# Kernel tuning notes

Hardware: AMD Instinct MI355X
Metric: run time of the kernel (lower is better)

## Reference

```python
import jax, jax.numpy as jnp
import numpy as np

N_NODES = 100000
N_EDGES = 1600000
DIM = 128
N_LAYERS = 3
N_GRAPHS = 512
BN_EPS = 1e-5


def setup_inputs() -> dict:
    key = jax.random.key(0)
    ks = jax.random.split(key, 8)
    x = jax.random.normal(ks[0], (N_NODES, DIM), dtype=jnp.float32)
    edge_index = jax.random.randint(ks[1], (2, N_EDGES), 0, N_NODES)
    batch = jnp.sort(jax.random.randint(ks[2], (N_NODES,), 0, N_GRAPHS))
    s = 1.0 / np.sqrt(DIM).astype(np.float32)
    # GIN MLP per layer: Linear(DIM->DIM), ReLU, Linear(DIM->DIM); stacked over layers
    W1 = jax.random.normal(ks[3], (N_LAYERS, DIM, DIM), dtype=jnp.float32) * s
    b1 = jnp.zeros((N_LAYERS, DIM), jnp.float32)
    W2 = jax.random.normal(ks[4], (N_LAYERS, DIM, DIM), dtype=jnp.float32) * s
    b2 = jnp.zeros((N_LAYERS, DIM), jnp.float32)
    # BatchNorm1d affine params
    gamma = jnp.ones((N_LAYERS, DIM), jnp.float32)
    beta = jnp.zeros((N_LAYERS, DIM), jnp.float32)
    return dict(x=x, edge_index=edge_index, batch=batch,
                W1=W1, b1=b1, W2=W2, b2=b2, gamma=gamma, beta=beta)


def reference(x, edge_index, batch, W1, b1, W2, b2, gamma, beta):
    src, dst = edge_index[0], edge_index[1]
    n = x.shape[0]
    z = x
    zs = []
    for l in range(N_LAYERS):
        # GINConv (eps=0): h_i = MLP((1+eps)*z_i + sum_{j in N(i)} z_j)
        agg = jax.ops.segment_sum(z[src], dst, num_segments=n)  # scatter-add messages
        h = agg + z
        h = jnp.maximum(h @ W1[l] + b1[l], 0.0) @ W2[l] + b2[l]
        h = jnp.maximum(h, 0.0)  # F.relu
        # BatchNorm1d (training-mode batch statistics, biased variance)
        mu = h.mean(axis=0)
        var = h.var(axis=0)
        z = (h - mu) * jax.lax.rsqrt(var + BN_EPS) * gamma[l] + beta[l]
        zs.append(z)
    gs = [jax.ops.segment_sum(zl, batch, num_segments=N_GRAPHS) for zl in zs]
    z_out = jnp.concatenate(zs, axis=1)   # [N, L*DIM]
    g_out = jnp.concatenate(gs, axis=1)   # [G, L*DIM]
    return (z_out, g_out)
```

## Files before the change

### kernel.cpp

```cpp
#include <hip/hip_runtime.h>

#define N_NODES 100000
#define N_EDGES 1600000
#define DIM 128
#define NLAYERS 3
#define NGRAPHS 512
#define BN_EPS 1e-5f

#define RT 64
#define KC 32
#define XP 36
#define WP 132
#define HP 132

#define SCHUNK 512
#define SBLOCKS ((N_NODES + SCHUNK - 1) / SCHUNK)

__global__ __launch_bounds__(256) void hist_kernel(const int* __restrict__ dst,
                                                   int* __restrict__ deg) {
  for (int e = blockIdx.x * blockDim.x + threadIdx.x; e < N_EDGES;
       e += gridDim.x * blockDim.x)
    atomicAdd(&deg[dst[e]], 1);
}

__global__ __launch_bounds__(256) void partial_kernel(const int* __restrict__ deg,
                                                      int* __restrict__ bsum) {
  __shared__ int red[256];
  const int t = threadIdx.x;
  const int i0 = blockIdx.x * SCHUNK + 2 * t;
  int s = 0;
  if (i0 + 1 < N_NODES) {
    const int2 v = *(const int2*)(deg + i0);
    s = v.x + v.y;
  } else if (i0 < N_NODES) {
    s = deg[i0];
  }
  red[t] = s;
  __syncthreads();
  for (int off = 128; off > 0; off >>= 1) {
    if (t < off) red[t] += red[t + off];
    __syncthreads();
  }
  if (t == 0) bsum[blockIdx.x] = red[0];
}

__global__ __launch_bounds__(256) void bscan_kernel(const int* __restrict__ bsum,
                                                    int* __restrict__ boff,
                                                    int* __restrict__ row_ptr) {
  __shared__ int s[256];
  const int t = threadIdx.x;
  const int v = (t < SBLOCKS) ? bsum[t] : 0;
  s[t] = v;
  __syncthreads();
  for (int off = 1; off < 256; off <<= 1) {
    int u = (t >= off) ? s[t - off] : 0;
    __syncthreads();
    s[t] += u;
    __syncthreads();
  }
  if (t < SBLOCKS) boff[t] = s[t] - v;
  if (t == SBLOCKS - 1) row_ptr[N_NODES] = s[t];
}

__global__ __launch_bounds__(256) void emit_kernel(const int* __restrict__ deg,
                                                   const int* __restrict__ boff,
                                                   int* __restrict__ row_ptr,
                                                   int* __restrict__ cursor) {
  __shared__ int s[256];
  const int t = threadIdx.x;
  const int i0 = blockIdx.x * SCHUNK + 2 * t;
  int d0 = 0, d1 = 0;
  if (i0 + 1 < N_NODES) {
    const int2 v = *(const int2*)(deg + i0);
    d0 = v.x; d1 = v.y;
  } else if (i0 < N_NODES) {
    d0 = deg[i0];
  }
  const int pair = d0 + d1;
  s[t] = pair;
  __syncthreads();
  for (int off = 1; off < 256; off <<= 1) {
    int u = (t >= off) ? s[t - off] : 0;
    __syncthreads();
    s[t] += u;
    __syncthreads();
  }
  const int base = boff[blockIdx.x] + s[t] - pair;
  if (i0 + 1 < N_NODES) {
    const int2 rp = make_int2(base, base + d0);
    *(int2*)(row_ptr + i0) = rp;
    *(int2*)(cursor + i0) = rp;
  } else if (i0 < N_NODES) {
    row_ptr[i0] = base;
    cursor[i0] = base;
  }
}

__global__ __launch_bounds__(256) void fill_kernel(const int* __restrict__ src,
                                                   const int* __restrict__ dst,
                                                   int* __restrict__ cursor,
                                                   int* __restrict__ col) {
  for (int e = blockIdx.x * blockDim.x + threadIdx.x; e < N_EDGES;
       e += gridDim.x * blockDim.x) {
    const int d = dst[e];
    const int pos = atomicAdd(&cursor[d], 1);
    col[pos] = src[e];
  }
}

__global__ __launch_bounds__(256) void agg_kernel(const float* __restrict__ zin,
                                                  int zstride,
                                                  const int* __restrict__ row_ptr,
                                                  const int* __restrict__ col,
                                                  float* __restrict__ agg) {
  const int w = (blockIdx.x * 256 + threadIdx.x) >> 6;
  const int lane = threadIdx.x & 63;
  if (w >= N_NODES) return;
  const int start = row_ptr[w];
  const int end = row_ptr[w + 1];

  float2 acc = ((const float2*)(zin + (size_t)w * zstride))[lane];
  int j = start;
  for (; j + 8 <= end; j += 8) {
    const int c0 = col[j], c1 = col[j + 1], c2 = col[j + 2], c3 = col[j + 3];
    const int c4 = col[j + 4], c5 = col[j + 5], c6 = col[j + 6], c7 = col[j + 7];
    const float2 v0 = ((const float2*)(zin + (size_t)c0 * zstride))[lane];
    const float2 v1 = ((const float2*)(zin + (size_t)c1 * zstride))[lane];
    const float2 v2 = ((const float2*)(zin + (size_t)c2 * zstride))[lane];
    const float2 v3 = ((const float2*)(zin + (size_t)c3 * zstride))[lane];
    const float2 v4 = ((const float2*)(zin + (size_t)c4 * zstride))[lane];
    const float2 v5 = ((const float2*)(zin + (size_t)c5 * zstride))[lane];
    const float2 v6 = ((const float2*)(zin + (size_t)c6 * zstride))[lane];
    const float2 v7 = ((const float2*)(zin + (size_t)c7 * zstride))[lane];
    acc.x += ((v0.x + v1.x) + (v2.x + v3.x)) + ((v4.x + v5.x) + (v6.x + v7.x));
    acc.y += ((v0.y + v1.y) + (v2.y + v3.y)) + ((v4.y + v5.y) + (v6.y + v7.y));
  }
  for (; j + 4 <= end; j += 4) {
    const int c0 = col[j], c1 = col[j + 1], c2 = col[j + 2], c3 = col[j + 3];
    const float2 v0 = ((const float2*)(zin + (size_t)c0 * zstride))[lane];
    const float2 v1 = ((const float2*)(zin + (size_t)c1 * zstride))[lane];
    const float2 v2 = ((const float2*)(zin + (size_t)c2 * zstride))[lane];
    const float2 v3 = ((const float2*)(zin + (size_t)c3 * zstride))[lane];
    acc.x += (v0.x + v1.x) + (v2.x + v3.x);
    acc.y += (v0.y + v1.y) + (v2.y + v3.y);
  }
  for (; j < end; ++j) {
    const int c = col[j];
    const float2 v = ((const float2*)(zin + (size_t)c * zstride))[lane];
    acc.x += v.x;
    acc.y += v.y;
  }
  ((float2*)(agg + (size_t)w * DIM))[lane] = acc;
}

__global__ __launch_bounds__(256) void mlp_kernel(
    const float* __restrict__ X,
    const float* __restrict__ W1, const float* __restrict__ b1,
    const float* __restrict__ W2, const float* __restrict__ b2,
    float* __restrict__ out,
    int lcol,
    float* __restrict__ bnsum) {
  __shared__ float smem[32 * WP + RT * HP];
  float* Ws = smem;
  float* Xs = smem + 32 * WP;
  float* Hs = smem + 32 * WP;
  float* red = smem + 32 * WP;

  const int tid = threadIdx.x;
  const int cg = tid & 15, rg = tid >> 4;
  const int c0 = cg * 8, r0 = rg * 4;
  const int n0 = blockIdx.x * RT;

  float4 acc[4][2];
#pragma unroll
  for (int rr = 0; rr < 4; ++rr) {
    acc[rr][0] = make_float4(0.f, 0.f, 0.f, 0.f);
    acc[rr][1] = make_float4(0.f, 0.f, 0.f, 0.f);
  }

  for (int kc = 0; kc < DIM / KC; ++kc) {
    const int k0 = kc * KC;
    __syncthreads();
    {
      const int kk = tid >> 3, q = tid & 7;
      const float4* s = (const float4*)(W1 + (size_t)(k0 + kk) * DIM + q * 16);
      float4* d = (float4*)(Ws + kk * WP + q * 16);
      d[0] = s[0]; d[1] = s[1]; d[2] = s[2]; d[3] = s[3];
    }
    {
      const int i = tid >> 2, q = tid & 3;
      const int n = n0 + i;
      float4 v0 = make_float4(0, 0, 0, 0), v1 = v0;
      if (n < N_NODES) {
        const float4* s = (const float4*)(X + (size_t)n * DIM + k0 + q * 8);
        v0 = s[0]; v1 = s[1];
      }
      float4* d = (float4*)(Xs + i * XP + q * 8);
      d[0] = v0; d[1] = v1;
    }
    __syncthreads();
#pragma unroll 8
    for (int kk = 0; kk < KC; ++kk) {
      const float4 wA = *(const float4*)(Ws + kk * WP + c0);
      const float4 wB = *(const float4*)(Ws + kk * WP + c0 + 4);
#pragma unroll
      for (int rr = 0; rr < 4; ++rr) {
        const float a = Xs[(r0 + rr) * XP + kk];
        acc[rr][0].x = fmaf(a, wA.x, acc[rr][0].x);
        acc[rr][0].y = fmaf(a, wA.y, acc[rr][0].y);
        acc[rr][0].z = fmaf(a, wA.z, acc[rr][0].z);
        acc[rr][0].w = fmaf(a, wA.w, acc[rr][0].w);
        acc[rr][1].x = fmaf(a, wB.x, acc[rr][1].x);
        acc[rr][1].y = fmaf(a, wB.y, acc[rr][1].y);
        acc[rr][1].z = fmaf(a, wB.z, acc[rr][1].z);
        acc[rr][1].w = fmaf(a, wB.w, acc[rr][1].w);
      }
    }
  }

  const float4 b1A = *(const float4*)(b1 + c0);
  const float4 b1B = *(const float4*)(b1 + c0 + 4);
  __syncthreads();
#pragma unroll
  for (int rr = 0; rr < 4; ++rr) {
    float4 hA, hB;
    hA.x = fmaxf(acc[rr][0].x + b1A.x, 0.f);
    hA.y = fmaxf(acc[rr][0].y + b1A.y, 0.f);
    hA.z = fmaxf(acc[rr][0].z + b1A.z, 0.f);
    hA.w = fmaxf(acc[rr][0].w + b1A.w, 0.f);
    hB.x = fmaxf(acc[rr][1].x + b1B.x, 0.f);
    hB.y = fmaxf(acc[rr][1].y + b1B.y, 0.f);
    hB.z = fmaxf(acc[rr][1].z + b1B.z, 0.f);
    hB.w = fmaxf(acc[rr][1].w + b1B.w, 0.f);
    *(float4*)(Hs + (r0 + rr) * HP + c0) = hA;
    *(float4*)(Hs + (r0 + rr) * HP + c0 + 4) = hB;
    acc[rr][0] = make_float4(0.f, 0.f, 0.f, 0.f);
    acc[rr][1] = make_float4(0.f, 0.f, 0.f, 0.f);
  }

  for (int kc = 0; kc < DIM / KC; ++kc) {
    const int k0 = kc * KC;
    __syncthreads();
    {
      const int kk = tid >> 3, q = tid & 7;
      const float4* s = (const float4*)(W2 + (size_t)(k0 + kk) * DIM + q * 16);
      float4* d = (float4*)(Ws + kk * WP + q * 16);
      d[0] = s[0]; d[1] = s[1]; d[2] = s[2]; d[3] = s[3];
    }
    __syncthreads();
#pragma unroll 8
    for (int kk = 0; kk < KC; ++kk) {
      const float4 wA = *(const float4*)(Ws + kk * WP + c0);
      const float4 wB = *(const float4*)(Ws + kk * WP + c0 + 4);
#pragma unroll
      for (int rr = 0; rr < 4; ++rr) {
        const float a = Hs[(r0 + rr) * HP + k0 + kk];
        acc[rr][0].x = fmaf(a, wA.x, acc[rr][0].x);
        acc[rr][0].y = fmaf(a, wA.y, acc[rr][0].y);
        acc[rr][0].z = fmaf(a, wA.z, acc[rr][0].z);
        acc[rr][0].w = fmaf(a, wA.w, acc[rr][0].w);
        acc[rr][1].x = fmaf(a, wB.x, acc[rr][1].x);
        acc[rr][1].y = fmaf(a, wB.y, acc[rr][1].y);
        acc[rr][1].z = fmaf(a, wB.z, acc[rr][1].z);
        acc[rr][1].w = fmaf(a, wB.w, acc[rr][1].w);
      }
    }
  }

  const float4 b2A = *(const float4*)(b2 + c0);
  const float4 b2B = *(const float4*)(b2 + c0 + 4);
  float s[8], q2[8];
#pragma unroll
  for (int cc = 0; cc < 8; ++cc) { s[cc] = 0.f; q2[cc] = 0.f; }
#pragma unroll
  for (int rr = 0; rr < 4; ++rr) {
    const int n = n0 + r0 + rr;
    float4 hA, hB;
    hA.x = fmaxf(acc[rr][0].x + b2A.x, 0.f);
    hA.y = fmaxf(acc[rr][0].y + b2A.y, 0.f);
    hA.z = fmaxf(acc[rr][0].z + b2A.z, 0.f);
    hA.w = fmaxf(acc[rr][0].w + b2A.w, 0.f);
    hB.x = fmaxf(acc[rr][1].x + b2B.x, 0.f);
    hB.y = fmaxf(acc[rr][1].y + b2B.y, 0.f);
    hB.z = fmaxf(acc[rr][1].z + b2B.z, 0.f);
    hB.w = fmaxf(acc[rr][1].w + b2B.w, 0.f);
    if (n < N_NODES) {
      *(float4*)(out + (size_t)n * (NLAYERS * DIM) + lcol + c0) = hA;
      *(float4*)(out + (size_t)n * (NLAYERS * DIM) + lcol + c0 + 4) = hB;
      s[0] += hA.x; s[1] += hA.y; s[2] += hA.z; s[3] += hA.w;
      s[4] += hB.x; s[5] += hB.y; s[6] += hB.z; s[7] += hB.w;
      q2[0] += hA.x * hA.x; q2[1] += hA.y * hA.y;
      q2[2] += hA.z * hA.z; q2[3] += hA.w * hA.w;
      q2[4] += hB.x * hB.x; q2[5] += hB.y * hB.y;
      q2[6] += hB.z * hB.z; q2[7] += hB.w * hB.w;
    }
  }
  __syncthreads();
#pragma unroll
  for (int cc = 0; cc < 8; ++cc) red[rg * 128 + c0 + cc] = s[cc];
  __syncthreads();
  if (tid < 128) {
    float t = 0.f;
#pragma unroll
    for (int g = 0; g < 16; ++g) t += red[g * 128 + tid];
    unsafeAtomicAdd(&bnsum[tid], t);
  }
  __syncthreads();
#pragma unroll
  for (int cc = 0; cc < 8; ++cc) red[rg * 128 + c0 + cc] = q2[cc];
  __syncthreads();
  if (tid < 128) {
    float t = 0.f;
#pragma unroll
    for (int g = 0; g < 16; ++g) t += red[g * 128 + tid];
    unsafeAtomicAdd(&bnsum[128 + tid], t);
  }
}

__global__ __launch_bounds__(128) void bn_finalize_kernel(
    const float* __restrict__ bnsum, const float* __restrict__ gamma,
    const float* __restrict__ beta, float* __restrict__ bnfin) {
  const int c = threadIdx.x;
  const float inv_n = 1.f / (float)N_NODES;
  const float mu = bnsum[c] * inv_n;
  const float var = bnsum[128 + c] * inv_n - mu * mu;
  const float inv = rsqrtf(var + BN_EPS);
  const float sc = gamma[c] * inv;
  bnfin[c] = sc;
  bnfin[128 + c] = beta[c] - mu * sc;
}

__global__ __launch_bounds__(256) void bn_norm_kernel(float* __restrict__ zcol,
                                                      const float* __restrict__ bnfin) {
  const int idx = blockIdx.x * 256 + threadIdx.x;
  if (idx >= N_NODES * 32) return;
  const int n = idx >> 5, c4 = idx & 31;
  const float4 sc = ((const float4*)bnfin)[c4];
  const float4 sh = ((const float4*)(bnfin + 128))[c4];
  float4* p = (float4*)(zcol + (size_t)n * (NLAYERS * DIM)) + c4;
  float4 v = *p;
  v.x = fmaf(v.x, sc.x, sh.x);
  v.y = fmaf(v.y, sc.y, sh.y);
  v.z = fmaf(v.z, sc.z, sh.z);
  v.w = fmaf(v.w, sc.w, sh.w);
  *p = v;
}

__global__ __launch_bounds__(128) void pool_kernel(const float* __restrict__ zout,
                                                   const int* __restrict__ batch,
                                                   float* __restrict__ gout) {
  const int g = blockIdx.x / 3;
  const int chunk = blockIdx.x % 3;
  const int c = chunk * 128 + threadIdx.x;
  int lo = 0, hi = N_NODES;
  while (lo < hi) {
    const int m = (lo + hi) >> 1;
    if (batch[m] < g) lo = m + 1; else hi = m;
  }
  int lo2 = lo, hi2 = N_NODES;
  while (lo2 < hi2) {
    const int m = (lo2 + hi2) >> 1;
    if (batch[m] < g + 1) lo2 = m + 1; else hi2 = m;
  }
  float acc = 0.f;
  for (int n = lo; n < lo2; ++n) acc += zout[(size_t)n * (NLAYERS * DIM) + c];
  gout[(size_t)g * (NLAYERS * DIM) + c] = acc;
}

extern "C" void kernel_launch(void* const* d_in, const int* in_sizes, int n_in,
                              void* d_out, int out_size, void* d_ws, size_t ws_size,
                              hipStream_t stream) {
  const float* x = (const float*)d_in[0];
  const int* ei = (const int*)d_in[1];
  const int* src = ei;
  const int* dst = ei + N_EDGES;
  const int* batch = (const int*)d_in[2];
  const float* W1 = (const float*)d_in[3];
  const float* b1 = (const float*)d_in[4];
  const float* W2 = (const float*)d_in[5];
  const float* b2 = (const float*)d_in[6];
  const float* gamma = (const float*)d_in[7];
  const float* beta = (const float*)d_in[8];
  float* out = (float*)d_out;
  float* gout = out + (size_t)N_NODES * NLAYERS * DIM;

  char* ws = (char*)d_ws;
  size_t off = 0;
  auto alloc = [&](size_t bytes) -> void* {
    off = (off + 511) & ~(size_t)511;
    void* p = ws + off;
    off += bytes;
    return p;
  };
  int* row_ptr = (int*)alloc((N_NODES + 1) * sizeof(int));
  int* cursor = (int*)alloc(N_NODES * sizeof(int));
  int* deg = (int*)alloc(N_NODES * sizeof(int));
  int* col = (int*)alloc(N_EDGES * sizeof(int));
  int* bsum = (int*)alloc(SBLOCKS * sizeof(int));
  int* boff = (int*)alloc(SBLOCKS * sizeof(int));
  float* agg = (float*)alloc((size_t)N_NODES * DIM * sizeof(float));
  float* bnsum = (float*)alloc(NLAYERS * 256 * sizeof(float));
  float* bnfin = (float*)alloc(NLAYERS * 256 * sizeof(float));

  hipMemsetAsync(deg, 0, N_NODES * sizeof(int), stream);
  hipMemsetAsync(bnsum, 0, NLAYERS * 256 * sizeof(float), stream);

  hist_kernel<<<2048, 256, 0, stream>>>(dst, deg);
  partial_kernel<<<SBLOCKS, 256, 0, stream>>>(deg, bsum);
  bscan_kernel<<<1, 256, 0, stream>>>(bsum, boff, row_ptr);
  emit_kernel<<<SBLOCKS, 256, 0, stream>>>(deg, boff, row_ptr, cursor);
  fill_kernel<<<2048, 256, 0, stream>>>(src, dst, cursor, col);

  for (int l = 0; l < NLAYERS; ++l) {
    const float* zin = (l == 0) ? x : (out + (size_t)(l - 1) * DIM);
    const int zstride = (l == 0) ? DIM : NLAYERS * DIM;
    agg_kernel<<<(N_NODES * 64 + 255) / 256, 256, 0, stream>>>(zin, zstride,
                                                               row_ptr, col, agg);
    mlp_kernel<<<(N_NODES + RT - 1) / RT, 256, 0, stream>>>(
        agg, W1 + (size_t)l * DIM * DIM, b1 + (size_t)l * DIM,
        W2 + (size_t)l * DIM * DIM, b2 + (size_t)l * DIM, out, l * DIM,
        bnsum + l * 256);
    bn_finalize_kernel<<<1, 128, 0, stream>>>(bnsum + l * 256, gamma + l * DIM,
                                              beta + l * DIM, bnfin + l * 256);
    bn_norm_kernel<<<(N_NODES * 32 + 255) / 256, 256, 0, stream>>>(
        out + (size_t)l * DIM, bnfin + l * 256);
  }
  pool_kernel<<<NGRAPHS * 3, 128, 0, stream>>>(out, batch, gout);
}
```

Before: 1.159 ms.

## Use bf16x3 split MFMA for GIN MLP with pre-split weights

Replaces the fp32 FMA register-tiled MLP with MFMA 16x16x32 bf16 matrix instructions. Inputs and hidden activations are split into hi/lo bf16 pairs and multiplied with three MFMAs, which approximates fp32 accuracy. A new prologue kernel pre-splits W1/W2 into a transposed, padded bf16 layout so each k-chunk can be copied straight into LDS. The aim is to cut MLP compute time, at the cost of extra conversion work, a larger LDS footprint and a small loss of precision relative to fp32.

```diff
diff --git a/kernel.cpp b/kernel.cpp
--- a/kernel.cpp
+++ b/kernel.cpp
@@ -7,14 +7,23 @@
 #define NGRAPHS 512
 #define BN_EPS 1e-5f
 
-#define RT 64
-#define KC 32
-#define XP 36
-#define WP 132
-#define HP 132
-
 #define SCHUNK 512
 #define SBLOCKS ((N_NODES + SCHUNK - 1) / SCHUNK)
+
+#define WPL 5120
+#define WCH 10240
+#define LSTRIDE 81920
+
+typedef __attribute__((ext_vector_type(8))) short short8;
+typedef __attribute__((ext_vector_type(4))) float f32x4;
+
+__device__ __forceinline__ unsigned f2b(float f) {
+  unsigned u = __float_as_uint(f);
+  return (u + 0x7FFFu + ((u >> 16) & 1u)) >> 16;
+}
+__device__ __forceinline__ float b2f(unsigned hw) {
+  return __uint_as_float(hw << 16);
+}
 
 __global__ __launch_bounds__(256) void hist_kernel(const int* __restrict__ dst,
                                                    int* __restrict__ deg) {
@@ -106,6 +115,24 @@
     const int pos = atomicAdd(&cursor[d], 1);
     col[pos] = src[e];
   }
+}
+
+__global__ __launch_bounds__(256) void wcvt_kernel(const float* __restrict__ W1,
+                                                   const float* __restrict__ W2,
+                                                   ushort* __restrict__ wsplit) {
+  const int id = blockIdx.x * 256 + threadIdx.x;
+  const int n = id & 127;
+  const int kk = (id >> 7) & 31;
+  const int kc = (id >> 12) & 3;
+  const int p = (id >> 14) & 1;
+  const int l = id >> 15;
+  const float* src = p ? W2 : W1;
+  const float v = src[(size_t)l * 16384 + (kc * 32 + kk) * 128 + n];
+  const unsigned hi = f2b(v);
+  const unsigned lo = f2b(v - b2f(hi));
+  ushort* dst = wsplit + (size_t)((l * 2 + p) * 4 + kc) * WCH + n * 40 + kk;
+  dst[0] = (ushort)hi;
+  dst[WPL] = (ushort)lo;
 }
 
 __global__ __launch_bounds__(256) void agg_kernel(const float* __restrict__ zin,
@@ -155,149 +182,105 @@
 
 __global__ __launch_bounds__(256) void mlp_kernel(
     const float* __restrict__ X,
-    const float* __restrict__ W1, const float* __restrict__ b1,
-    const float* __restrict__ W2, const float* __restrict__ b2,
+    const ushort* __restrict__ Wsp,
+    const float* __restrict__ b1,
+    const float* __restrict__ b2,
     float* __restrict__ out,
     int lcol,
     float* __restrict__ bnsum) {
-  __shared__ float smem[32 * WP + RT * HP];
-  float* Ws = smem;
-  float* Xs = smem + 32 * WP;
-  float* Hs = smem + 32 * WP;
-  float* red = smem + 32 * WP;
+  __shared__ __align__(16) ushort smem[2 * 64 * 136 + WCH];
+  ushort* Xh = smem;
+  ushort* Xl = smem + 64 * 136;
+  ushort* Wc = smem + 2 * 64 * 136;
+  float* red = (float*)smem;
 
   const int tid = threadIdx.x;
-  const int cg = tid & 15, rg = tid >> 4;
-  const int c0 = cg * 8, r0 = rg * 4;
-  const int n0 = blockIdx.x * RT;
-
-  float4 acc[4][2];
-#pragma unroll
-  for (int rr = 0; rr < 4; ++rr) {
-    acc[rr][0] = make_float4(0.f, 0.f, 0.f, 0.f);
-    acc[rr][1] = make_float4(0.f, 0.f, 0.f, 0.f);
-  }
-
-  for (int kc = 0; kc < DIM / KC; ++kc) {
-    const int k0 = kc * KC;
-    __syncthreads();
-    {
-      const int kk = tid >> 3, q = tid & 7;
-      const float4* s = (const float4*)(W1 + (size_t)(k0 + kk) * DIM + q * 16);
-      float4* d = (float4*)(Ws + kk * WP + q * 16);
-      d[0] = s[0]; d[1] = s[1]; d[2] = s[2]; d[3] = s[3];
-    }
-    {
-      const int i = tid >> 2, q = tid & 3;
-      const int n = n0 + i;
-      float4 v0 = make_float4(0, 0, 0, 0), v1 = v0;
-      if (n < N_NODES) {
-        const float4* s = (const float4*)(X + (size_t)n * DIM + k0 + q * 8);
-        v0 = s[0]; v1 = s[1];
+  const int l = tid & 63, wv = tid >> 6;
+  const int lr = l & 15, lg = l >> 4;
+  const int n0 = blockIdx.x * 64;
+
+  for (int i = tid; i < 64 * 32; i += 256) {
+    const int row = i >> 5, c4 = (i & 31) * 4;
+    float4 v = make_float4(0.f, 0.f, 0.f, 0.f);
+    if (n0 + row < N_NODES) v = *(const float4*)(X + (size_t)(n0 + row) * 128 + c4);
+    ushort4 hi, lo;
+    hi.x = (ushort)f2b(v.x); lo.x = (ushort)f2b(v.x - b2f(hi.x));
+    hi.y = (ushort)f2b(v.y); lo.y = (ushort)f2b(v.y - b2f(hi.y));
+    hi.z = (ushort)f2b(v.z); lo.z = (ushort)f2b(v.z - b2f(hi.z));
+    hi.w = (ushort)f2b(v.w); lo.w = (ushort)f2b(v.w - b2f(hi.w));
+    *(ushort4*)(Xh + row * 136 + c4) = hi;
+    *(ushort4*)(Xl + row * 136 + c4) = lo;
+  }
+
+  f32x4 acc[8];
+#pragma unroll
+  for (int p = 0; p < 2; ++p) {
+#pragma unroll
+    for (int nt = 0; nt < 8; ++nt) acc[nt] = {0.f, 0.f, 0.f, 0.f};
+#pragma unroll
+    for (int kc = 0; kc < 4; ++kc) {
+      __syncthreads();
+      {
+        const uint4* wsrc = (const uint4*)(Wsp + (size_t)(p * 4 + kc) * WCH);
+        for (int i = tid; i < WCH / 8; i += 256) ((uint4*)Wc)[i] = wsrc[i];
       }
-      float4* d = (float4*)(Xs + i * XP + q * 8);
-      d[0] = v0; d[1] = v1;
-    }
-    __syncthreads();
-#pragma unroll 8
-    for (int kk = 0; kk < KC; ++kk) {
-      const float4 wA = *(const float4*)(Ws + kk * WP + c0);
-      const float4 wB = *(const float4*)(Ws + kk * WP + c0 + 4);
-#pragma unroll
-      for (int rr = 0; rr < 4; ++rr) {
-        const float a = Xs[(r0 + rr) * XP + kk];
-        acc[rr][0].x = fmaf(a, wA.x, acc[rr][0].x);
-        acc[rr][0].y = fmaf(a, wA.y, acc[rr][0].y);
-        acc[rr][0].z = fmaf(a, wA.z, acc[rr][0].z);
-        acc[rr][0].w = fmaf(a, wA.w, acc[rr][0].w);
-        acc[rr][1].x = fmaf(a, wB.x, acc[rr][1].x);
-        acc[rr][1].y = fmaf(a, wB.y, acc[rr][1].y);
-        acc[rr][1].z = fmaf(a, wB.z, acc[rr][1].z);
-        acc[rr][1].w = fmaf(a, wB.w, acc[rr][1].w);
+      __syncthreads();
+      const short8 ah = *(const short8*)(Xh + (wv * 16 + lr) * 136 + kc * 32 + lg * 8);
+      const short8 al = *(const short8*)(Xl + (wv * 16 + lr) * 136 + kc * 32 + lg * 8);
+#pragma unroll
+      for (int nt = 0; nt < 8; ++nt) {
+        const short8 bh = *(const short8*)(Wc + (nt * 16 + lr) * 40 + lg * 8);
+        const short8 bl = *(const short8*)(Wc + WPL + (nt * 16 + lr) * 40 + lg * 8);
+        acc[nt] = __builtin_amdgcn_mfma_f32_16x16x32_bf16(ah, bh, acc[nt], 0, 0, 0);
+        acc[nt] = __builtin_amdgcn_mfma_f32_16x16x32_bf16(al, bh, acc[nt], 0, 0, 0);
+        acc[nt] = __builtin_amdgcn_mfma_f32_16x16x32_bf16(ah, bl, acc[nt], 0, 0, 0);
       }
     }
-  }
-
-  const float4 b1A = *(const float4*)(b1 + c0);
-  const float4 b1B = *(const float4*)(b1 + c0 + 4);
-  __syncthreads();
-#pragma unroll
-  for (int rr = 0; rr < 4; ++rr) {
-    float4 hA, hB;
-    hA.x = fmaxf(acc[rr][0].x + b1A.x, 0.f);
-    hA.y = fmaxf(acc[rr][0].y + b1A.y, 0.f);
-    hA.z = fmaxf(acc[rr][0].z + b1A.z, 0.f);
-    hA.w = fmaxf(acc[rr][0].w + b1A.w, 0.f);
-    hB.x = fmaxf(acc[rr][1].x + b1B.x, 0.f);
-    hB.y = fmaxf(acc[rr][1].y + b1B.y, 0.f);
-    hB.z = fmaxf(acc[rr][1].z + b1B.z, 0.f);
-    hB.w = fmaxf(acc[rr][1].w + b1B.w, 0.f);
-    *(float4*)(Hs + (r0 + rr) * HP + c0) = hA;
-    *(float4*)(Hs + (r0 + rr) * HP + c0 + 4) = hB;
-    acc[rr][0] = make_float4(0.f, 0.f, 0.f, 0.f);
-    acc[rr][1] = make_float4(0.f, 0.f, 0.f, 0.f);
-  }
-
-  for (int kc = 0; kc < DIM / KC; ++kc) {
-    const int k0 = kc * KC;
-    __syncthreads();
-    {
-      const int kk = tid >> 3, q = tid & 7;
-      const float4* s = (const float4*)(W2 + (size_t)(k0 + kk) * DIM + q * 16);
-      float4* d = (float4*)(Ws + kk * WP + q * 16);
-      d[0] = s[0]; d[1] = s[1]; d[2] = s[2]; d[3] = s[3];
-    }
-    __syncthreads();
-#pragma unroll 8
-    for (int kk = 0; kk < KC; ++kk) {
-      const float4 wA = *(const float4*)(Ws + kk * WP + c0);
-      const float4 wB = *(const float4*)(Ws + kk * WP + c0 + 4);
-#pragma unroll
-      for (int rr = 0; rr < 4; ++rr) {
-        const float a = Hs[(r0 + rr) * HP + k0 + kk];
-        acc[rr][0].x = fmaf(a, wA.x, acc[rr][0].x);
-        acc[rr][0].y = fmaf(a, wA.y, acc[rr][0].y);
-        acc[rr][0].z = fmaf(a, wA.z, acc[rr][0].z);
-        acc[rr][0].w = fmaf(a, wA.w, acc[rr][0].w);
-        acc[rr][1].x = fmaf(a, wB.x, acc[rr][1].x);
-        acc[rr][1].y = fmaf(a, wB.y, acc[rr][1].y);
-        acc[rr][1].z = fmaf(a, wB.z, acc[rr][1].z);
-        acc[rr][1].w = fmaf(a, wB.w, acc[rr][1].w);
+    if (p == 0) {
+      __syncthreads();
+      float b1v[8];
+#pragma unroll
+      for (int nt = 0; nt < 8; ++nt) b1v[nt] = b1[nt * 16 + lr];
+#pragma unroll
+      for (int nt = 0; nt < 8; ++nt) {
+#pragma unroll
+        for (int r = 0; r < 4; ++r) {
+          const float h = fmaxf(acc[nt][r] + b1v[nt], 0.f);
+          const unsigned hi = f2b(h);
+          const unsigned lo = f2b(h - b2f(hi));
+          Xh[(wv * 16 + lg * 4 + r) * 136 + nt * 16 + lr] = (ushort)hi;
+          Xl[(wv * 16 + lg * 4 + r) * 136 + nt * 16 + lr] = (ushort)lo;
+        }
       }
     }
   }
 
-  const float4 b2A = *(const float4*)(b2 + c0);
-  const float4 b2B = *(const float4*)(b2 + c0 + 4);
   float s[8], q2[8];
-#pragma unroll
-  for (int cc = 0; cc < 8; ++cc) { s[cc] = 0.f; q2[cc] = 0.f; }
-#pragma unroll
-  for (int rr = 0; rr < 4; ++rr) {
-    const int n = n0 + r0 + rr;
-    float4 hA, hB;
-    hA.x = fmaxf(acc[rr][0].x + b2A.x, 0.f);
-    hA.y = fmaxf(acc[rr][0].y + b2A.y, 0.f);
-    hA.z = fmaxf(acc[rr][0].z + b2A.z, 0.f);
-    hA.w = fmaxf(acc[rr][0].w + b2A.w, 0.f);
-    hB.x = fmaxf(acc[rr][1].x + b2B.x, 0.f);
-    hB.y = fmaxf(acc[rr][1].y + b2B.y, 0.f);
-    hB.z = fmaxf(acc[rr][1].z + b2B.z, 0.f);
-    hB.w = fmaxf(acc[rr][1].w + b2B.w, 0.f);
-    if (n < N_NODES) {
-      *(float4*)(out + (size_t)n * (NLAYERS * DIM) + lcol + c0) = hA;
-      *(float4*)(out + (size_t)n * (NLAYERS * DIM) + lcol + c0 + 4) = hB;
-      s[0] += hA.x; s[1] += hA.y; s[2] += hA.z; s[3] += hA.w;
-      s[4] += hB.x; s[5] += hB.y; s[6] += hB.z; s[7] += hB.w;
-      q2[0] += hA.x * hA.x; q2[1] += hA.y * hA.y;
-      q2[2] += hA.z * hA.z; q2[3] += hA.w * hA.w;
-      q2[4] += hB.x * hB.x; q2[5] += hB.y * hB.y;
-      q2[6] += hB.z * hB.z; q2[7] += hB.w * hB.w;
+  {
+    float b2v[8];
+#pragma unroll
+    for (int nt = 0; nt < 8; ++nt) b2v[nt] = b2[nt * 16 + lr];
+#pragma unroll
+    for (int nt = 0; nt < 8; ++nt) { s[nt] = 0.f; q2[nt] = 0.f; }
+#pragma unroll
+    for (int nt = 0; nt < 8; ++nt) {
+#pragma unroll
+      for (int r = 0; r < 4; ++r) {
+        const int n = n0 + wv * 16 + lg * 4 + r;
+        const float h = fmaxf(acc[nt][r] + b2v[nt], 0.f);
+        if (n < N_NODES) {
+          out[(size_t)n * (NLAYERS * DIM) + lcol + nt * 16 + lr] = h;
+          s[nt] += h;
+          q2[nt] += h * h;
+        }
+      }
     }
   }
   __syncthreads();
-#pragma unroll
-  for (int cc = 0; cc < 8; ++cc) red[rg * 128 + c0 + cc] = s[cc];
+
+  const int rg = tid >> 4, cb = tid & 15;
+#pragma unroll
+  for (int nt = 0; nt < 8; ++nt) red[rg * 128 + nt * 16 + cb] = s[nt];
   __syncthreads();
   if (tid < 128) {
     float t = 0.f;
@@ -307,7 +290,7 @@
   }
   __syncthreads();
 #pragma unroll
-  for (int cc = 0; cc < 8; ++cc) red[rg * 128 + c0 + cc] = q2[cc];
+  for (int nt = 0; nt < 8; ++nt) red[rg * 128 + nt * 16 + cb] = q2[nt];
   __syncthreads();
   if (tid < 128) {
     float t = 0.f;
@@ -399,6 +382,7 @@
   int* bsum = (int*)alloc(SBLOCKS * sizeof(int));
   int* boff = (int*)alloc(SBLOCKS * sizeof(int));
   float* agg = (float*)alloc((size_t)N_NODES * DIM * sizeof(float));
+  ushort* wsplit = (ushort*)alloc((size_t)NLAYERS * LSTRIDE * sizeof(ushort));
   float* bnsum = (float*)alloc(NLAYERS * 256 * sizeof(float));
   float* bnfin = (float*)alloc(NLAYERS * 256 * sizeof(float));
 
@@ -410,16 +394,16 @@
   bscan_kernel<<<1, 256, 0, stream>>>(bsum, boff, row_ptr);
   emit_kernel<<<SBLOCKS, 256, 0, stream>>>(deg, boff, row_ptr, cursor);
   fill_kernel<<<2048, 256, 0, stream>>>(src, dst, cursor, col);
+  wcvt_kernel<<<384, 256, 0, stream>>>(W1, W2, wsplit);
 
   for (int l = 0; l < NLAYERS; ++l) {
     const float* zin = (l == 0) ? x : (out + (size_t)(l - 1) * DIM);
     const int zstride = (l == 0) ? DIM : NLAYERS * DIM;
     agg_kernel<<<(N_NODES * 64 + 255) / 256, 256, 0, stream>>>(zin, zstride,
                                                                row_ptr, col, agg);
-    mlp_kernel<<<(N_NODES + RT - 1) / RT, 256, 0, stream>>>(
-        agg, W1 + (size_t)l * DIM * DIM, b1 + (size_t)l * DIM,
-        W2 + (size_t)l * DIM * DIM, b2 + (size_t)l * DIM, out, l * DIM,
-        bnsum + l * 256);
+    mlp_kernel<<<(N_NODES + 63) / 64, 256, 0, stream>>>(
+        agg, wsplit + (size_t)l * LSTRIDE, b1 + (size_t)l * DIM,
+        b2 + (size_t)l * DIM, out, l * DIM, bnsum + l * 256);
     bn_finalize_kernel<<<1, 128, 0, stream>>>(bnsum + l * 256, gamma + l * DIM,
                                               beta + l * DIM, bnfin + l * 256);
     bn_norm_kernel<<<(N_NODES * 32 + 255) / 256, 256, 0, stream>>>(
```

After: 1.172 ms. No clear change (+1.1%).
